# Kernel optimization log

Hardware: AMD Instinct MI355X
Metric: run time of the kernel (lower is better)

The kernel has to match this reference:

```python
import jax, jax.numpy as jnp
import numpy as np

NUM_LAYERS = 4
HIDDEN = 32
INPUT = 2
B = 16384
T = 64


def setup_inputs() -> dict:
    key = jax.random.key(0)
    ks = jax.random.split(key, 8)
    s = 1.0 / np.sqrt(HIDDEN)  # PyTorch LSTM default init scale
    return {
        "x": jax.random.normal(ks[0], (B, 3, T), dtype=jnp.float32),
        "W_ih0": jax.random.uniform(ks[1], (4 * HIDDEN, INPUT), minval=-s, maxval=s, dtype=jnp.float32),
        "W_ih": jax.random.uniform(ks[2], (NUM_LAYERS - 1, 4 * HIDDEN, HIDDEN), minval=-s, maxval=s, dtype=jnp.float32),
        "W_hh": jax.random.uniform(ks[3], (NUM_LAYERS, 4 * HIDDEN, HIDDEN), minval=-s, maxval=s, dtype=jnp.float32),
        "b_ih": jax.random.uniform(ks[4], (NUM_LAYERS, 4 * HIDDEN), minval=-s, maxval=s, dtype=jnp.float32),
        "b_hh": jax.random.uniform(ks[5], (NUM_LAYERS, 4 * HIDDEN), minval=-s, maxval=s, dtype=jnp.float32),
        "W_lin": jax.random.uniform(ks[6], (1, HIDDEN), minval=-s, maxval=s, dtype=jnp.float32),
        "b_lin": jax.random.uniform(ks[7], (1,), minval=-s, maxval=s, dtype=jnp.float32),
    }


def _lstm_cell(inp, h, c, Wih, Whh, b):
    # inp: [B, in_dim]; h, c: [B, H]; Wih: [4H, in_dim]; Whh: [4H, H]; b: [4H]
    gates = inp @ Wih.T + h @ Whh.T + b  # [B, 4H]
    i, f, g, o = jnp.split(gates, 4, axis=-1)  # PyTorch gate order: i, f, g, o
    i = jax.nn.sigmoid(i)
    f = jax.nn.sigmoid(f)
    g = jnp.tanh(g)
    o = jax.nn.sigmoid(o)
    c_new = f * c + i * g
    h_new = o * jnp.tanh(c_new)
    return h_new, c_new


def reference(x, W_ih0, W_ih, W_hh, b_ih, b_hh, W_lin, b_lin):
    # x: [B, 3, T]; channel 2 (id) is discarded, as in the original forward.
    feats = x[:, :2, :]                         # [B, 2, T]
    xs = jnp.transpose(feats, (2, 0, 1))        # [T, B, 2]
    bsz = x.shape[0]
    h0 = jnp.zeros((NUM_LAYERS, bsz, HIDDEN), dtype=x.dtype)
    c0 = jnp.zeros((NUM_LAYERS, bsz, HIDDEN), dtype=x.dtype)
    bias = b_ih + b_hh  # [L, 4H]

    def step(carry, xt):
        h, c = carry  # each [L, B, H]
        inp = xt
        hs, cs = [], []
        for l in range(NUM_LAYERS):
            Wih = W_ih0 if l == 0 else W_ih[l - 1]
            h_new, c_new = _lstm_cell(inp, h[l], c[l], Wih, W_hh[l], bias[l])
            hs.append(h_new)
            cs.append(c_new)
            inp = h_new
        return (jnp.stack(hs), jnp.stack(cs)), None

    (h, c), _ = jax.lax.scan(step, (h0, c0), xs)
    # last timestep's top-layer output -> linear -> sigmoid -> squeeze to [B]
    out = jax.nn.sigmoid(h[-1] @ W_lin.T + b_lin)  # [B, 1]
    return out.squeeze(-1)
```

## Files before the change

kernel.cpp:

```cpp
#include <hip/hip_runtime.h>

typedef float  f32x4  __attribute__((ext_vector_type(4)));
typedef float  f32x2  __attribute__((ext_vector_type(2)));
typedef short  bf16x8 __attribute__((ext_vector_type(8)));

#define TWOLOG2E   2.8853900817779268f
#define NLOG2E    -1.4426950408889634f
#define NTWOLOG2E -2.8853900817779268f

__device__ __forceinline__ unsigned short f2b(float f) {
    unsigned int u = __builtin_bit_cast(unsigned int, f);
    u += 0x7fffu + ((u >> 16) & 1u);
    return (unsigned short)(u >> 16);
}
__device__ __forceinline__ float b2f(unsigned short s) {
    unsigned int u = ((unsigned int)s) << 16;
    return __builtin_bit_cast(float, u);
}
__device__ __forceinline__ unsigned int pk2(float lo, float hi) {
#if __has_builtin(__builtin_amdgcn_cvt_pk_bf16_f32)
    typedef __bf16 bf16x2 __attribute__((ext_vector_type(2)));
    bf16x2 p = __builtin_amdgcn_cvt_pk_bf16_f32(lo, hi);
    return __builtin_bit_cast(unsigned int, p);
#else
    return (unsigned int)f2b(lo) | ((unsigned int)f2b(hi) << 16);
#endif
}
__device__ __forceinline__ float frcp(float x) { return __builtin_amdgcn_rcpf(x); }
__device__ __forceinline__ float fex2(float x) { return __builtin_amdgcn_exp2f(x); }

__global__ __launch_bounds__(256, 1)
void lstm_mfma(const float* __restrict__ xg,  const float* __restrict__ Wih0,
               const float* __restrict__ Wih, const float* __restrict__ Whh,
               const float* __restrict__ bih, const float* __restrict__ bhh,
               const float* __restrict__ Wlin,const float* __restrict__ blin,
               float* __restrict__ out) {
    __shared__ unsigned int hb[16 * 1024] __attribute__((aligned(16)));
    __shared__ unsigned int xb[64 * 64];

    const int tid  = threadIdx.x;
    const int wv   = __builtin_amdgcn_readfirstlane(tid >> 6);
    const int lane = tid & 63;
    const int m    = lane & 15;
    const int q    = lane >> 4;
    const int row0 = blockIdx.x * 64;

    for (int i = tid; i < 4096; i += 256) {
        int r = i >> 6, t = i & 63;
        float x0 = xg[(size_t)(row0 + r) * 192 + t];
        float x1 = xg[(size_t)(row0 + r) * 192 + 64 + t];
        xb[t * 64 + r] = pk2(x0, x1);
    }

    bf16x8 afr[2][8];
    f32x4  cbq[8];
#pragma unroll
    for (int g = 0; g < 8; ++g) {
        const int   u_m  = 8 * (m >> 2) + 2 * (g & 3) + (m & 1);
        const int   gt_m = 2 * (g >> 2) + ((m >> 1) & 1);
        const int   rowG = gt_m * 32 + u_m;
        const float sc   = (gt_m == 2) ? NTWOLOG2E : NLOG2E;
        {
            float w[8];
            if (wv == 0) {
#pragma unroll
                for (int jj = 0; jj < 8; ++jj) w[jj] = 0.0f;
                if (q == 0) { w[0] = Wih0[rowG * 2]; w[1] = Wih0[rowG * 2 + 1]; }
            } else {
                const float* src = Wih + (wv - 1) * 4096 + rowG * 32 + q * 8;
#pragma unroll
                for (int jj = 0; jj < 8; ++jj) w[jj] = src[jj];
            }
            bf16x8 fr;
#pragma unroll
            for (int jj = 0; jj < 8; ++jj) fr[jj] = (short)f2b(w[jj] * sc);
            afr[0][g] = fr;
        }
        {
            const float* src = Whh + wv * 4096 + rowG * 32 + q * 8;
            bf16x8 fr;
#pragma unroll
            for (int jj = 0; jj < 8; ++jj) fr[jj] = (short)f2b(src[jj] * sc);
            afr[1][g] = fr;
        }
        f32x4 c4;
#pragma unroll
        for (int r = 0; r < 4; ++r) {
            const int   u_r  = 8 * q + 2 * (g & 3) + (r & 1);
            const int   gt_r = 2 * (g >> 2) + ((r >> 1) & 1);
            const float scr  = (gt_r == 2) ? NTWOLOG2E : NLOG2E;
            c4[r] = (bih[wv * 128 + gt_r * 32 + u_r] + bhh[wv * 128 + gt_r * 32 + u_r]) * scr;
        }
        cbq[g] = c4;
    }

    bf16x8 hreg[4];
#pragma unroll
    for (int tt = 0; tt < 4; ++tt) {
        union { unsigned int u[4]; bf16x8 v; } z;
        z.u[0] = 0u; z.u[1] = 0u; z.u[2] = 0u; z.u[3] = 0u;
        hreg[tt] = z.v;
    }
    f32x2 cp2[4][4];
#pragma unroll
    for (int tt = 0; tt < 4; ++tt)
#pragma unroll
        for (int j = 0; j < 4; ++j) cp2[tt][j] = (f32x2){0.0f, 0.0f};

    __syncthreads();

    auto chain = [&](f32x2 ai, f32x2 af, f32x2 ag, f32x2 ao, f32x2& cpr) -> f32x2 {
        const f32x2 one = {1.0f, 1.0f};
        const f32x2 c2l = {TWOLOG2E, TWOLOG2E};
        const f32x2 n2l = {NTWOLOG2E, NTWOLOG2E};
        f32x2 ei = {fex2(ai.x), fex2(ai.y)};
        f32x2 ef = {fex2(af.x), fex2(af.y)};
        f32x2 eg = {fex2(ag.x), fex2(ag.y)};
        f32x2 eo = {fex2(ao.x), fex2(ao.y)};
        f32x2 apf = one + ef;
        f32x2 p1  = (one + ei) * (one + eg);
        f32x2 Dc  = p1 * apf;
        f32x2 R_  = {frcp(Dc.x), frcp(Dc.y)};
        f32x2 egp = __builtin_elementwise_fma(eg, c2l, n2l);
        f32x2 t1  = egp * apf;
        f32x2 t2  = __builtin_elementwise_fma(cpr, p1, t1);
        f32x2 cn  = t2 * R_;
        cpr = cn;
        f32x2 ec  = {fex2(cn.x), fex2(cn.y)};
        f32x2 Dh  = (one + eo) * (one + ec);
        f32x2 Rh  = {frcp(Dh.x), frcp(Dh.y)};
        return (one - ec) * Rh;
    };

    auto cell_step = [&](int t, const unsigned int* pin, unsigned int* pout) {
#pragma unroll
        for (int tt = 0; tt < 4; ++tt) {
            bf16x8 bin;
            if (wv == 0) {
                unsigned int xd = xb[t * 64 + tt * 16 + m];
                union { unsigned int u[4]; bf16x8 v; } au;
                au.u[0] = (q == 0) ? xd : 0u; au.u[1] = 0u; au.u[2] = 0u; au.u[3] = 0u;
                bin = au.v;
            } else {
                bin = *(const bf16x8*)(pin + tt * 256 + lane * 4);
            }
            f32x4 acc[8];
#pragma unroll
            for (int g = 0; g < 8; ++g) {
                acc[g] = __builtin_amdgcn_mfma_f32_16x16x32_bf16(afr[0][g], bin, cbq[g], 0, 0, 0);
                acc[g] = __builtin_amdgcn_mfma_f32_16x16x32_bf16(afr[1][g], hreg[tt], acc[g], 0, 0, 0);
            }
            union { unsigned int u[4]; bf16x8 v; } hn;
#pragma unroll
            for (int j = 0; j < 4; ++j) {
                f32x2 ai = (f32x2)__builtin_shufflevector(acc[j],     acc[j],     0, 1);
                f32x2 af = (f32x2)__builtin_shufflevector(acc[j],     acc[j],     2, 3);
                f32x2 ag = (f32x2)__builtin_shufflevector(acc[4 + j], acc[4 + j], 0, 1);
                f32x2 ao = (f32x2)__builtin_shufflevector(acc[4 + j], acc[4 + j], 2, 3);
                f32x2 hh = chain(ai, af, ag, ao, cp2[tt][j]);
                hn.u[j] = pk2(hh.x, hh.y);
            }
            hreg[tt] = hn.v;
            *(bf16x8*)(pout + tt * 256 + lane * 4) = hn.v;
        }
    };

    for (int S = 0; S < 35; ++S) {
        const int t0 = 2 * (S - wv);
        if (t0 >= 0 && t0 <= 62) {
            const int p  = S & 1;
            const int pb = p ^ 1;
            unsigned int*       Lc0 = hb + ((wv * 2 + p ) * 2    ) * 1024;
            unsigned int*       Lc1 = Lc0 + 1024;
            const int           lb  = (wv > 0) ? (wv - 1) : 0;
            const unsigned int* Dp0 = hb + ((lb * 2 + pb) * 2    ) * 1024;
            const unsigned int* Dp1 = Dp0 + 1024;

            cell_step(t0,     Dp0, Lc0);
            cell_step(t0 + 1, Dp1, Lc1);
        }
        __syncthreads();
    }

    if (tid < 64) {
        const unsigned int* h3 = hb + ((3 * 2 + 0) * 2 + 1) * 1024;
        const int tt = tid >> 4, mm = tid & 15;
        float s = blin[0];
#pragma unroll
        for (int qq = 0; qq < 4; ++qq)
#pragma unroll
            for (int j = 0; j < 4; ++j) {
                unsigned int w2 = h3[tt * 256 + (qq * 16 + mm) * 4 + j];
                const int u0 = 8 * qq + 2 * j;
                s += Wlin[u0]     * b2f((unsigned short)(w2 & 0xffffu));
                s += Wlin[u0 + 1] * b2f((unsigned short)(w2 >> 16));
            }
        out[row0 + tid] = frcp(1.0f + fex2(s * NLOG2E));
    }
}

extern "C" void kernel_launch(void* const* d_in, const int* in_sizes, int n_in,
                              void* d_out, int out_size, void* d_ws, size_t ws_size,
                              hipStream_t stream) {
    const float* x    = (const float*)d_in[0];
    const float* Wih0 = (const float*)d_in[1];
    const float* Wih  = (const float*)d_in[2];
    const float* Whh  = (const float*)d_in[3];
    const float* bih  = (const float*)d_in[4];
    const float* bhh  = (const float*)d_in[5];
    const float* Wlin = (const float*)d_in[6];
    const float* blin = (const float*)d_in[7];
    float* out = (float*)d_out;

    lstm_mfma<<<256, 256, 0, stream>>>(x, Wih0, Wih, Whh, bih, bhh, Wlin, blin, out);
}
```

Measured before the change: 250.7 us.

## Give each wave all four layers for its own batch slice instead of layer pipelining

Before, each wave owned one LSTM layer and passed hidden states between layers through shared memory in a wavefront schedule with a block barrier every stage. Now each wave keeps the weights for all four layers in registers and runs the full layer stack over time for its own 16 batch rows. This removes the shared-memory hidden-state traffic, the per-stage barriers and the pipeline fill and drain bubbles. In exchange it raises register pressure sharply (weights and biases for all layers held per lane) and gives up the overlap of independent layers across waves, so each wave's work becomes one long serial dependency chain.

Result: no change. 255.0 us (+1.7%).

```diff
diff --git a/kernel.cpp b/kernel.cpp
--- a/kernel.cpp
+++ b/kernel.cpp
@@ -35,7 +35,6 @@
                const float* __restrict__ bih, const float* __restrict__ bhh,
                const float* __restrict__ Wlin,const float* __restrict__ blin,
                float* __restrict__ out) {
-    __shared__ unsigned int hb[16 * 1024] __attribute__((aligned(16)));
     __shared__ unsigned int xb[64 * 64];
 
     const int tid  = threadIdx.x;
@@ -52,150 +51,138 @@
         xb[t * 64 + r] = pk2(x0, x1);
     }
 
-    bf16x8 afr[2][8];
-    f32x4  cbq[8];
+    unsigned int w01[8];
+    bf16x8 ain[3][8];
+    bf16x8 arc[4][8];
+    f32x4  cbq[4][8];
 #pragma unroll
     for (int g = 0; g < 8; ++g) {
         const int   u_m  = 8 * (m >> 2) + 2 * (g & 3) + (m & 1);
         const int   gt_m = 2 * (g >> 2) + ((m >> 1) & 1);
         const int   rowG = gt_m * 32 + u_m;
         const float sc   = (gt_m == 2) ? NTWOLOG2E : NLOG2E;
-        {
-            float w[8];
-            if (wv == 0) {
-#pragma unroll
-                for (int jj = 0; jj < 8; ++jj) w[jj] = 0.0f;
-                if (q == 0) { w[0] = Wih0[rowG * 2]; w[1] = Wih0[rowG * 2 + 1]; }
-            } else {
-                const float* src = Wih + (wv - 1) * 4096 + rowG * 32 + q * 8;
-#pragma unroll
-                for (int jj = 0; jj < 8; ++jj) w[jj] = src[jj];
+        w01[g] = (unsigned int)f2b(Wih0[rowG * 2] * sc)
+               | ((unsigned int)f2b(Wih0[rowG * 2 + 1] * sc) << 16);
+#pragma unroll
+        for (int l = 0; l < 3; ++l) {
+            const float* src = Wih + l * 4096 + rowG * 32 + q * 8;
+            bf16x8 fr;
+#pragma unroll
+            for (int jj = 0; jj < 8; ++jj) fr[jj] = (short)f2b(src[jj] * sc);
+            ain[l][g] = fr;
+        }
+#pragma unroll
+        for (int l = 0; l < 4; ++l) {
+            const float* src = Whh + l * 4096 + rowG * 32 + q * 8;
+            bf16x8 fr;
+#pragma unroll
+            for (int jj = 0; jj < 8; ++jj) fr[jj] = (short)f2b(src[jj] * sc);
+            arc[l][g] = fr;
+        }
+#pragma unroll
+        for (int l = 0; l < 4; ++l) {
+            f32x4 c4;
+#pragma unroll
+            for (int r = 0; r < 4; ++r) {
+                const int   u_r  = 8 * q + 2 * (g & 3) + (r & 1);
+                const int   gt_r = 2 * (g >> 2) + ((r >> 1) & 1);
+                const float scr  = (gt_r == 2) ? NTWOLOG2E : NLOG2E;
+                c4[r] = (bih[l * 128 + gt_r * 32 + u_r] + bhh[l * 128 + gt_r * 32 + u_r]) * scr;
             }
-            bf16x8 fr;
-#pragma unroll
-            for (int jj = 0; jj < 8; ++jj) fr[jj] = (short)f2b(w[jj] * sc);
-            afr[0][g] = fr;
-        }
-        {
-            const float* src = Whh + wv * 4096 + rowG * 32 + q * 8;
-            bf16x8 fr;
-#pragma unroll
-            for (int jj = 0; jj < 8; ++jj) fr[jj] = (short)f2b(src[jj] * sc);
-            afr[1][g] = fr;
-        }
-        f32x4 c4;
-#pragma unroll
-        for (int r = 0; r < 4; ++r) {
-            const int   u_r  = 8 * q + 2 * (g & 3) + (r & 1);
-            const int   gt_r = 2 * (g >> 2) + ((r >> 1) & 1);
-            const float scr  = (gt_r == 2) ? NTWOLOG2E : NLOG2E;
-            c4[r] = (bih[wv * 128 + gt_r * 32 + u_r] + bhh[wv * 128 + gt_r * 32 + u_r]) * scr;
-        }
-        cbq[g] = c4;
-    }
-
-    bf16x8 hreg[4];
-#pragma unroll
-    for (int tt = 0; tt < 4; ++tt) {
+            cbq[l][g] = c4;
+        }
+    }
+
+    bf16x8 h[4];
+#pragma unroll
+    for (int l = 0; l < 4; ++l) {
         union { unsigned int u[4]; bf16x8 v; } z;
         z.u[0] = 0u; z.u[1] = 0u; z.u[2] = 0u; z.u[3] = 0u;
-        hreg[tt] = z.v;
-    }
-    f32x2 cp2[4][4];
-#pragma unroll
-    for (int tt = 0; tt < 4; ++tt)
-#pragma unroll
-        for (int j = 0; j < 4; ++j) cp2[tt][j] = (f32x2){0.0f, 0.0f};
+        h[l] = z.v;
+    }
+    f32x2 cp[4][4];
+#pragma unroll
+    for (int l = 0; l < 4; ++l)
+#pragma unroll
+        for (int j = 0; j < 4; ++j) cp[l][j] = (f32x2){0.0f, 0.0f};
 
     __syncthreads();
 
-    auto chain = [&](f32x2 ai, f32x2 af, f32x2 ag, f32x2 ao, f32x2& cpr) -> f32x2 {
-        const f32x2 one = {1.0f, 1.0f};
-        const f32x2 c2l = {TWOLOG2E, TWOLOG2E};
-        const f32x2 n2l = {NTWOLOG2E, NTWOLOG2E};
-        f32x2 ei = {fex2(ai.x), fex2(ai.y)};
-        f32x2 ef = {fex2(af.x), fex2(af.y)};
-        f32x2 eg = {fex2(ag.x), fex2(ag.y)};
-        f32x2 eo = {fex2(ao.x), fex2(ao.y)};
-        f32x2 apf = one + ef;
-        f32x2 p1  = (one + ei) * (one + eg);
-        f32x2 Dc  = p1 * apf;
-        f32x2 R_  = {frcp(Dc.x), frcp(Dc.y)};
-        f32x2 egp = __builtin_elementwise_fma(eg, c2l, n2l);
-        f32x2 t1  = egp * apf;
-        f32x2 t2  = __builtin_elementwise_fma(cpr, p1, t1);
-        f32x2 cn  = t2 * R_;
-        cpr = cn;
-        f32x2 ec  = {fex2(cn.x), fex2(cn.y)};
-        f32x2 Dh  = (one + eo) * (one + ec);
-        f32x2 Rh  = {frcp(Dh.x), frcp(Dh.y)};
-        return (one - ec) * Rh;
+    const f32x2 one = {1.0f, 1.0f};
+    const f32x2 c2l = {TWOLOG2E, TWOLOG2E};
+    const f32x2 n2l = {NTWOLOG2E, NTWOLOG2E};
+
+    auto cell = [&](f32x4 (&acc)[8], bf16x8& hslot, f32x2 (&cps)[4]) {
+        union { unsigned int u[4]; bf16x8 v; } hn;
+#pragma unroll
+        for (int j = 0; j < 4; ++j) {
+            f32x2 ai = (f32x2)__builtin_shufflevector(acc[j],     acc[j],     0, 1);
+            f32x2 af = (f32x2)__builtin_shufflevector(acc[j],     acc[j],     2, 3);
+            f32x2 ag = (f32x2)__builtin_shufflevector(acc[4 + j], acc[4 + j], 0, 1);
+            f32x2 ao = (f32x2)__builtin_shufflevector(acc[4 + j], acc[4 + j], 2, 3);
+            f32x2 ei = {fex2(ai.x), fex2(ai.y)};
+            f32x2 ef = {fex2(af.x), fex2(af.y)};
+            f32x2 eg = {fex2(ag.x), fex2(ag.y)};
+            f32x2 eo = {fex2(ao.x), fex2(ao.y)};
+            f32x2 apf = one + ef;
+            f32x2 p1  = (one + ei) * (one + eg);
+            f32x2 Dc  = p1 * apf;
+            f32x2 R_  = {frcp(Dc.x), frcp(Dc.y)};
+            f32x2 egp = __builtin_elementwise_fma(eg, c2l, n2l);
+            f32x2 t2  = __builtin_elementwise_fma(cps[j], p1, egp * apf);
+            f32x2 cn  = t2 * R_;
+            cps[j] = cn;
+            f32x2 ec  = {fex2(cn.x), fex2(cn.y)};
+            f32x2 Dh  = (one + eo) * (one + ec);
+            f32x2 Rh  = {frcp(Dh.x), frcp(Dh.y)};
+            f32x2 hh  = (one - ec) * Rh;
+            hn.u[j] = pk2(hh.x, hh.y);
+        }
+        hslot = hn.v;
     };
 
-    auto cell_step = [&](int t, const unsigned int* pin, unsigned int* pout) {
-#pragma unroll
-        for (int tt = 0; tt < 4; ++tt) {
-            bf16x8 bin;
-            if (wv == 0) {
-                unsigned int xd = xb[t * 64 + tt * 16 + m];
+#pragma unroll 1
+    for (int t = 0; t < 64; ++t) {
+        {
+            unsigned int xd = xb[t * 64 + wv * 16 + m];
+            union { unsigned int u[4]; bf16x8 v; } bu;
+            bu.u[0] = (q == 0) ? xd : 0u; bu.u[1] = 0u; bu.u[2] = 0u; bu.u[3] = 0u;
+            f32x4 acc[8];
+#pragma unroll
+            for (int g = 0; g < 8; ++g) {
                 union { unsigned int u[4]; bf16x8 v; } au;
-                au.u[0] = (q == 0) ? xd : 0u; au.u[1] = 0u; au.u[2] = 0u; au.u[3] = 0u;
-                bin = au.v;
-            } else {
-                bin = *(const bf16x8*)(pin + tt * 256 + lane * 4);
+                au.u[0] = (q == 0) ? w01[g] : 0u; au.u[1] = 0u; au.u[2] = 0u; au.u[3] = 0u;
+                acc[g] = __builtin_amdgcn_mfma_f32_16x16x32_bf16(au.v, bu.v, cbq[0][g], 0, 0, 0);
+                acc[g] = __builtin_amdgcn_mfma_f32_16x16x32_bf16(arc[0][g], h[0], acc[g], 0, 0, 0);
             }
+            cell(acc, h[0], cp[0]);
+        }
+#pragma unroll
+        for (int l = 1; l < 4; ++l) {
             f32x4 acc[8];
 #pragma unroll
             for (int g = 0; g < 8; ++g) {
-                acc[g] = __builtin_amdgcn_mfma_f32_16x16x32_bf16(afr[0][g], bin, cbq[g], 0, 0, 0);
-                acc[g] = __builtin_amdgcn_mfma_f32_16x16x32_bf16(afr[1][g], hreg[tt], acc[g], 0, 0, 0);
+                acc[g] = __builtin_amdgcn_mfma_f32_16x16x32_bf16(ain[l - 1][g], h[l - 1], cbq[l][g], 0, 0, 0);
+                acc[g] = __builtin_amdgcn_mfma_f32_16x16x32_bf16(arc[l][g], h[l], acc[g], 0, 0, 0);
             }
-            union { unsigned int u[4]; bf16x8 v; } hn;
-#pragma unroll
-            for (int j = 0; j < 4; ++j) {
-                f32x2 ai = (f32x2)__builtin_shufflevector(acc[j],     acc[j],     0, 1);
-                f32x2 af = (f32x2)__builtin_shufflevector(acc[j],     acc[j],     2, 3);
-                f32x2 ag = (f32x2)__builtin_shufflevector(acc[4 + j], acc[4 + j], 0, 1);
-                f32x2 ao = (f32x2)__builtin_shufflevector(acc[4 + j], acc[4 + j], 2, 3);
-                f32x2 hh = chain(ai, af, ag, ao, cp2[tt][j]);
-                hn.u[j] = pk2(hh.x, hh.y);
-            }
-            hreg[tt] = hn.v;
-            *(bf16x8*)(pout + tt * 256 + lane * 4) = hn.v;
-        }
-    };
-
-    for (int S = 0; S < 35; ++S) {
-        const int t0 = 2 * (S - wv);
-        if (t0 >= 0 && t0 <= 62) {
-            const int p  = S & 1;
-            const int pb = p ^ 1;
-            unsigned int*       Lc0 = hb + ((wv * 2 + p ) * 2    ) * 1024;
-            unsigned int*       Lc1 = Lc0 + 1024;
-            const int           lb  = (wv > 0) ? (wv - 1) : 0;
-            const unsigned int* Dp0 = hb + ((lb * 2 + pb) * 2    ) * 1024;
-            const unsigned int* Dp1 = Dp0 + 1024;
-
-            cell_step(t0,     Dp0, Lc0);
-            cell_step(t0 + 1, Dp1, Lc1);
-        }
-        __syncthreads();
-    }
-
-    if (tid < 64) {
-        const unsigned int* h3 = hb + ((3 * 2 + 0) * 2 + 1) * 1024;
-        const int tt = tid >> 4, mm = tid & 15;
-        float s = blin[0];
-#pragma unroll
-        for (int qq = 0; qq < 4; ++qq)
-#pragma unroll
-            for (int j = 0; j < 4; ++j) {
-                unsigned int w2 = h3[tt * 256 + (qq * 16 + mm) * 4 + j];
-                const int u0 = 8 * qq + 2 * j;
-                s += Wlin[u0]     * b2f((unsigned short)(w2 & 0xffffu));
-                s += Wlin[u0 + 1] * b2f((unsigned short)(w2 >> 16));
-            }
-        out[row0 + tid] = frcp(1.0f + fex2(s * NLOG2E));
+            cell(acc, h[l], cp[l]);
+        }
+    }
+
+    {
+        union { unsigned int u[4]; bf16x8 v; } h3; h3.v = h[3];
+        float s = 0.0f;
+#pragma unroll
+        for (int j = 0; j < 4; ++j) {
+            unsigned int w2 = h3.u[j];
+            const int u0 = 8 * q + 2 * j;
+            s += Wlin[u0]     * b2f((unsigned short)(w2 & 0xffffu));
+            s += Wlin[u0 + 1] * b2f((unsigned short)(w2 >> 16));
+        }
+        s += __shfl_xor(s, 16, 64);
+        s += __shfl_xor(s, 32, 64);
+        if (lane < 16)
+            out[row0 + wv * 16 + m] = frcp(1.0f + fex2((s + blin[0]) * NLOG2E));
     }
 }
 
```

## Shrink per-block batch to 16 rows and launch 1024 blocks with 4 per CU

Applied to the files above, without the earlier changes.

Each block now handles 16 batch rows instead of 64, and the grid grows from 256 to 1024 blocks. Launch bounds allow 4 blocks per CU. The input-to-hidden weight fragments move from registers into shared memory, x is read straight from global each step, and the hidden-state buffer shrinks accordingly. The final linear layer is computed from registers using a lane shuffle reduction. The aim is to fill the whole GPU and overlap several wavefront pipelines per CU so the serial recurrence latency is hidden. The cost is extra LDS reads for weights and uncoalesced global reads of x inside the time loop.

After: 233.4 us. 6.9% less time.

```diff
diff --git a/kernel.cpp b/kernel.cpp
--- a/kernel.cpp
+++ b/kernel.cpp
@@ -29,30 +29,47 @@
 __device__ __forceinline__ float frcp(float x) { return __builtin_amdgcn_rcpf(x); }
 __device__ __forceinline__ float fex2(float x) { return __builtin_amdgcn_exp2f(x); }
 
-__global__ __launch_bounds__(256, 1)
+__global__ __launch_bounds__(256, 4)
 void lstm_mfma(const float* __restrict__ xg,  const float* __restrict__ Wih0,
                const float* __restrict__ Wih, const float* __restrict__ Whh,
                const float* __restrict__ bih, const float* __restrict__ bhh,
                const float* __restrict__ Wlin,const float* __restrict__ blin,
                float* __restrict__ out) {
-    __shared__ unsigned int hb[16 * 1024] __attribute__((aligned(16)));
-    __shared__ unsigned int xb[64 * 64];
+    __shared__ unsigned int wlds[3 * 8 * 64 * 4] __attribute__((aligned(16)));
+    __shared__ unsigned int w0lds[8 * 64];
+    __shared__ unsigned int hb[12 * 256] __attribute__((aligned(16)));
 
     const int tid  = threadIdx.x;
     const int wv   = __builtin_amdgcn_readfirstlane(tid >> 6);
     const int lane = tid & 63;
     const int m    = lane & 15;
     const int q    = lane >> 4;
-    const int row0 = blockIdx.x * 64;
-
-    for (int i = tid; i < 4096; i += 256) {
-        int r = i >> 6, t = i & 63;
-        float x0 = xg[(size_t)(row0 + r) * 192 + t];
-        float x1 = xg[(size_t)(row0 + r) * 192 + 64 + t];
-        xb[t * 64 + r] = pk2(x0, x1);
-    }
-
-    bf16x8 afr[2][8];
+    const int row0 = blockIdx.x * 16;
+
+    for (int idx = tid; idx < 1536; idx += 256) {
+        const int l1 = idx >> 9, g = (idx >> 6) & 7, ln = idx & 63;
+        const int mm = ln & 15, qq = ln >> 4;
+        const int   u_m  = 8 * (mm >> 2) + 2 * (g & 3) + (mm & 1);
+        const int   gt_m = 2 * (g >> 2) + ((mm >> 1) & 1);
+        const int   rowG = gt_m * 32 + u_m;
+        const float sc   = (gt_m == 2) ? NTWOLOG2E : NLOG2E;
+        const float* src = Wih + l1 * 4096 + rowG * 32 + qq * 8;
+        unsigned int* dst = wlds + idx * 4;
+#pragma unroll
+        for (int w2 = 0; w2 < 4; ++w2)
+            dst[w2] = pk2(src[2 * w2] * sc, src[2 * w2 + 1] * sc);
+    }
+    for (int idx = tid; idx < 512; idx += 256) {
+        const int g = idx >> 6, ln = idx & 63;
+        const int mm = ln & 15, qq = ln >> 4;
+        const int   u_m  = 8 * (mm >> 2) + 2 * (g & 3) + (mm & 1);
+        const int   gt_m = 2 * (g >> 2) + ((mm >> 1) & 1);
+        const int   rowG = gt_m * 32 + u_m;
+        const float sc   = (gt_m == 2) ? NTWOLOG2E : NLOG2E;
+        w0lds[idx] = (qq == 0) ? pk2(Wih0[rowG * 2] * sc, Wih0[rowG * 2 + 1] * sc) : 0u;
+    }
+
+    bf16x8 afr1[8];
     f32x4  cbq[8];
 #pragma unroll
     for (int g = 0; g < 8; ++g) {
@@ -60,29 +77,11 @@
         const int   gt_m = 2 * (g >> 2) + ((m >> 1) & 1);
         const int   rowG = gt_m * 32 + u_m;
         const float sc   = (gt_m == 2) ? NTWOLOG2E : NLOG2E;
-        {
-            float w[8];
-            if (wv == 0) {
-#pragma unroll
-                for (int jj = 0; jj < 8; ++jj) w[jj] = 0.0f;
-                if (q == 0) { w[0] = Wih0[rowG * 2]; w[1] = Wih0[rowG * 2 + 1]; }
-            } else {
-                const float* src = Wih + (wv - 1) * 4096 + rowG * 32 + q * 8;
-#pragma unroll
-                for (int jj = 0; jj < 8; ++jj) w[jj] = src[jj];
-            }
-            bf16x8 fr;
-#pragma unroll
-            for (int jj = 0; jj < 8; ++jj) fr[jj] = (short)f2b(w[jj] * sc);
-            afr[0][g] = fr;
-        }
-        {
-            const float* src = Whh + wv * 4096 + rowG * 32 + q * 8;
-            bf16x8 fr;
-#pragma unroll
-            for (int jj = 0; jj < 8; ++jj) fr[jj] = (short)f2b(src[jj] * sc);
-            afr[1][g] = fr;
-        }
+        const float* src = Whh + wv * 4096 + rowG * 32 + q * 8;
+        bf16x8 fr;
+#pragma unroll
+        for (int jj = 0; jj < 8; ++jj) fr[jj] = (short)f2b(src[jj] * sc);
+        afr1[g] = fr;
         f32x4 c4;
 #pragma unroll
         for (int r = 0; r < 4; ++r) {
@@ -94,75 +93,81 @@
         cbq[g] = c4;
     }
 
-    bf16x8 hreg[4];
-#pragma unroll
-    for (int tt = 0; tt < 4; ++tt) {
+    bf16x8 hreg;
+    {
         union { unsigned int u[4]; bf16x8 v; } z;
         z.u[0] = 0u; z.u[1] = 0u; z.u[2] = 0u; z.u[3] = 0u;
-        hreg[tt] = z.v;
-    }
-    f32x2 cp2[4][4];
-#pragma unroll
-    for (int tt = 0; tt < 4; ++tt)
-#pragma unroll
-        for (int j = 0; j < 4; ++j) cp2[tt][j] = (f32x2){0.0f, 0.0f};
+        hreg = z.v;
+    }
+    f32x2 cp2[4];
+#pragma unroll
+    for (int j = 0; j < 4; ++j) cp2[j] = (f32x2){0.0f, 0.0f};
 
     __syncthreads();
 
-    auto chain = [&](f32x2 ai, f32x2 af, f32x2 ag, f32x2 ao, f32x2& cpr) -> f32x2 {
-        const f32x2 one = {1.0f, 1.0f};
-        const f32x2 c2l = {TWOLOG2E, TWOLOG2E};
-        const f32x2 n2l = {NTWOLOG2E, NTWOLOG2E};
-        f32x2 ei = {fex2(ai.x), fex2(ai.y)};
-        f32x2 ef = {fex2(af.x), fex2(af.y)};
-        f32x2 eg = {fex2(ag.x), fex2(ag.y)};
-        f32x2 eo = {fex2(ao.x), fex2(ao.y)};
-        f32x2 apf = one + ef;
-        f32x2 p1  = (one + ei) * (one + eg);
-        f32x2 Dc  = p1 * apf;
-        f32x2 R_  = {frcp(Dc.x), frcp(Dc.y)};
-        f32x2 egp = __builtin_elementwise_fma(eg, c2l, n2l);
-        f32x2 t1  = egp * apf;
-        f32x2 t2  = __builtin_elementwise_fma(cpr, p1, t1);
-        f32x2 cn  = t2 * R_;
-        cpr = cn;
-        f32x2 ec  = {fex2(cn.x), fex2(cn.y)};
-        f32x2 Dh  = (one + eo) * (one + ec);
-        f32x2 Rh  = {frcp(Dh.x), frcp(Dh.y)};
-        return (one - ec) * Rh;
-    };
-
-    auto cell_step = [&](int t, const unsigned int* pin, unsigned int* pout) {
-#pragma unroll
-        for (int tt = 0; tt < 4; ++tt) {
-            bf16x8 bin;
+    const f32x2 one = {1.0f, 1.0f};
+    const f32x2 c2l = {TWOLOG2E, TWOLOG2E};
+    const f32x2 n2l = {NTWOLOG2E, NTWOLOG2E};
+
+    auto cell_step = [&](int t, int sidx_in, int sidx_out) {
+        bf16x8 bin;
+        if (wv == 0) {
+            union { unsigned int u[4]; bf16x8 v; } bu;
+            bu.u[0] = 0u; bu.u[1] = 0u; bu.u[2] = 0u; bu.u[3] = 0u;
+            if (q == 0) {
+                float x0 = xg[(size_t)(row0 + m) * 192 + t];
+                float x1 = xg[(size_t)(row0 + m) * 192 + 64 + t];
+                bu.u[0] = pk2(x0, x1);
+            }
+            bin = bu.v;
+        } else {
+            bin = *(const bf16x8*)(hb + sidx_in * 256 + lane * 4);
+        }
+
+        union { unsigned int u[4]; bf16x8 v; } hn;
+#pragma unroll
+        for (int j = 0; j < 4; ++j) {
+            f32x4 accA, accB;
             if (wv == 0) {
-                unsigned int xd = xb[t * 64 + tt * 16 + m];
-                union { unsigned int u[4]; bf16x8 v; } au;
-                au.u[0] = (q == 0) ? xd : 0u; au.u[1] = 0u; au.u[2] = 0u; au.u[3] = 0u;
-                bin = au.v;
+                union { unsigned int u[4]; bf16x8 v; } au, av;
+                au.u[0] = w0lds[j * 64 + lane];       au.u[1] = 0u; au.u[2] = 0u; au.u[3] = 0u;
+                av.u[0] = w0lds[(4 + j) * 64 + lane]; av.u[1] = 0u; av.u[2] = 0u; av.u[3] = 0u;
+                accA = __builtin_amdgcn_mfma_f32_16x16x32_bf16(au.v, bin, cbq[j],     0, 0, 0);
+                accB = __builtin_amdgcn_mfma_f32_16x16x32_bf16(av.v, bin, cbq[4 + j], 0, 0, 0);
             } else {
-                bin = *(const bf16x8*)(pin + tt * 256 + lane * 4);
+                const bf16x8 fa = *(const bf16x8*)(wlds + (((wv - 1) * 8 + j)     * 64 + lane) * 4);
+                const bf16x8 fb = *(const bf16x8*)(wlds + (((wv - 1) * 8 + 4 + j) * 64 + lane) * 4);
+                accA = __builtin_amdgcn_mfma_f32_16x16x32_bf16(fa, bin, cbq[j],     0, 0, 0);
+                accB = __builtin_amdgcn_mfma_f32_16x16x32_bf16(fb, bin, cbq[4 + j], 0, 0, 0);
             }
-            f32x4 acc[8];
-#pragma unroll
-            for (int g = 0; g < 8; ++g) {
-                acc[g] = __builtin_amdgcn_mfma_f32_16x16x32_bf16(afr[0][g], bin, cbq[g], 0, 0, 0);
-                acc[g] = __builtin_amdgcn_mfma_f32_16x16x32_bf16(afr[1][g], hreg[tt], acc[g], 0, 0, 0);
-            }
-            union { unsigned int u[4]; bf16x8 v; } hn;
-#pragma unroll
-            for (int j = 0; j < 4; ++j) {
-                f32x2 ai = (f32x2)__builtin_shufflevector(acc[j],     acc[j],     0, 1);
-                f32x2 af = (f32x2)__builtin_shufflevector(acc[j],     acc[j],     2, 3);
-                f32x2 ag = (f32x2)__builtin_shufflevector(acc[4 + j], acc[4 + j], 0, 1);
-                f32x2 ao = (f32x2)__builtin_shufflevector(acc[4 + j], acc[4 + j], 2, 3);
-                f32x2 hh = chain(ai, af, ag, ao, cp2[tt][j]);
-                hn.u[j] = pk2(hh.x, hh.y);
-            }
-            hreg[tt] = hn.v;
-            *(bf16x8*)(pout + tt * 256 + lane * 4) = hn.v;
-        }
+            accA = __builtin_amdgcn_mfma_f32_16x16x32_bf16(afr1[j],     hreg, accA, 0, 0, 0);
+            accB = __builtin_amdgcn_mfma_f32_16x16x32_bf16(afr1[4 + j], hreg, accB, 0, 0, 0);
+
+            f32x2 ai = (f32x2)__builtin_shufflevector(accA, accA, 0, 1);
+            f32x2 af = (f32x2)__builtin_shufflevector(accA, accA, 2, 3);
+            f32x2 ag = (f32x2)__builtin_shufflevector(accB, accB, 0, 1);
+            f32x2 ao = (f32x2)__builtin_shufflevector(accB, accB, 2, 3);
+            f32x2 ei = {fex2(ai.x), fex2(ai.y)};
+            f32x2 ef = {fex2(af.x), fex2(af.y)};
+            f32x2 eg = {fex2(ag.x), fex2(ag.y)};
+            f32x2 eo = {fex2(ao.x), fex2(ao.y)};
+            f32x2 apf = one + ef;
+            f32x2 p1  = (one + ei) * (one + eg);
+            f32x2 Dc  = p1 * apf;
+            f32x2 R_  = {frcp(Dc.x), frcp(Dc.y)};
+            f32x2 egp = __builtin_elementwise_fma(eg, c2l, n2l);
+            f32x2 t2  = __builtin_elementwise_fma(cp2[j], p1, egp * apf);
+            f32x2 cn  = t2 * R_;
+            cp2[j] = cn;
+            f32x2 ec  = {fex2(cn.x), fex2(cn.y)};
+            f32x2 Dh  = (one + eo) * (one + ec);
+            f32x2 Rh  = {frcp(Dh.x), frcp(Dh.y)};
+            f32x2 hh  = (one - ec) * Rh;
+            hn.u[j] = pk2(hh.x, hh.y);
+        }
+        hreg = hn.v;
+        if (sidx_out >= 0)
+            *(bf16x8*)(hb + sidx_out * 256 + lane * 4) = hn.v;
     };
 
     for (int S = 0; S < 35; ++S) {
@@ -170,32 +175,28 @@
         if (t0 >= 0 && t0 <= 62) {
             const int p  = S & 1;
             const int pb = p ^ 1;
-            unsigned int*       Lc0 = hb + ((wv * 2 + p ) * 2    ) * 1024;
-            unsigned int*       Lc1 = Lc0 + 1024;
-            const int           lb  = (wv > 0) ? (wv - 1) : 0;
-            const unsigned int* Dp0 = hb + ((lb * 2 + pb) * 2    ) * 1024;
-            const unsigned int* Dp1 = Dp0 + 1024;
-
-            cell_step(t0,     Dp0, Lc0);
-            cell_step(t0 + 1, Dp1, Lc1);
+            const int si = (wv > 0) ? (((wv - 1) * 2 + pb) * 2) : -1;
+            const int so = (wv < 3) ? ((wv * 2 + p) * 2)        : -1;
+            cell_step(t0,     si,              so);
+            cell_step(t0 + 1, si < 0 ? -1 : si + 1, so < 0 ? -1 : so + 1);
         }
         __syncthreads();
     }
 
-    if (tid < 64) {
-        const unsigned int* h3 = hb + ((3 * 2 + 0) * 2 + 1) * 1024;
-        const int tt = tid >> 4, mm = tid & 15;
-        float s = blin[0];
-#pragma unroll
-        for (int qq = 0; qq < 4; ++qq)
-#pragma unroll
-            for (int j = 0; j < 4; ++j) {
-                unsigned int w2 = h3[tt * 256 + (qq * 16 + mm) * 4 + j];
-                const int u0 = 8 * qq + 2 * j;
-                s += Wlin[u0]     * b2f((unsigned short)(w2 & 0xffffu));
-                s += Wlin[u0 + 1] * b2f((unsigned short)(w2 >> 16));
-            }
-        out[row0 + tid] = frcp(1.0f + fex2(s * NLOG2E));
+    if (wv == 3) {
+        union { unsigned int u[4]; bf16x8 v; } h3; h3.v = hreg;
+        float s = 0.0f;
+#pragma unroll
+        for (int j = 0; j < 4; ++j) {
+            unsigned int w2 = h3.u[j];
+            const int u0 = 8 * q + 2 * j;
+            s += Wlin[u0]     * b2f((unsigned short)(w2 & 0xffffu));
+            s += Wlin[u0 + 1] * b2f((unsigned short)(w2 >> 16));
+        }
+        s += __shfl_xor(s, 16, 64);
+        s += __shfl_xor(s, 32, 64);
+        if (lane < 16)
+            out[row0 + m] = frcp(1.0f + fex2((s + blin[0]) * NLOG2E));
     }
 }
 
@@ -212,5 +213,5 @@
     const float* blin = (const float*)d_in[7];
     float* out = (float*)d_out;
 
-    lstm_mfma<<<256, 256, 0, stream>>>(x, Wih0, Wih, Whh, bih, bhh, Wlin, blin, out);
-}
+    lstm_mfma<<<1024, 256, 0, stream>>>(x, Wih0, Wih, Whh, bih, bhh, Wlin, blin, out);
+}
```
